# Optimization experiments

Hardware: AMD Instinct MI355X
Metric: run time of the kernel (lower is better)

Reference implementation:

```python
import jax, jax.numpy as jnp
import numpy as np
from jax import lax

WINDOW_SIZE = 11
SIGMA = 1.5
MAX_VAL = 1.0


def _gaussian_kernel_2d(window_size: int, sigma: float) -> jnp.ndarray:
    coords = jnp.arange(window_size, dtype=jnp.float32) - window_size // 2
    g = jnp.exp(-coords ** 2 / (2.0 * sigma ** 2))
    g = g / g.sum()
    k2d = jnp.outer(g, g)
    return k2d / k2d.sum()  # [W, W]


def _depthwise_conv(x: jnp.ndarray, k2d: jnp.ndarray) -> jnp.ndarray:
    # x: [B, C, H, W]; depthwise (groups=C) conv with SAME padding
    C = x.shape[1]
    ws = k2d.shape[0]
    kernel = jnp.broadcast_to(k2d[None, None], (C, 1, ws, ws)).astype(x.dtype)  # [C,1,ws,ws]
    pad = ws // 2
    return lax.conv_general_dilated(
        x, kernel,
        window_strides=(1, 1),
        padding=((pad, pad), (pad, pad)),
        dimension_numbers=('NCHW', 'OIHW', 'NCHW'),
        feature_group_count=C,
    )


def setup_inputs() -> dict:
    key = jax.random.key(0)
    k1, k2 = jax.random.split(key)
    B, C, H, W = 16, 3, 512, 512
    sr = jax.random.uniform(k1, (B, C, H, W), dtype=jnp.float32)
    hr = jax.random.uniform(k2, (B, C, H, W), dtype=jnp.float32)
    return {"sr": sr, "hr": hr}


def reference(sr, hr):
    c1 = (0.01 * MAX_VAL) ** 2
    c2 = (0.03 * MAX_VAL) ** 2
    k2d = _gaussian_kernel_2d(WINDOW_SIZE, SIGMA)

    mu1 = _depthwise_conv(sr, k2d)
    mu2 = _depthwise_conv(hr, k2d)
    mu1_sq = mu1 ** 2
    mu2_sq = mu2 ** 2
    mu1_mu2 = mu1 * mu2
    sigma1_sq = _depthwise_conv(sr * sr, k2d) - mu1_sq
    sigma2_sq = _depthwise_conv(hr * hr, k2d) - mu2_sq
    sigma12 = _depthwise_conv(sr * hr, k2d) - mu1_mu2

    ssim_map = (2 * mu1_mu2 + c1) * (2 * sigma12 + c2) / (
        (mu1_sq + mu2_sq + c1) * (sigma1_sq + sigma2_sq + c2) + 1e-12)
    return 1.0 - ssim_map.mean()
```

## Files before the change

### kernel.cpp

```cpp
#include <hip/hip_runtime.h>


typedef __attribute__((ext_vector_type(2))) float  f32x2;
typedef __attribute__((ext_vector_type(4))) float  f32x4;
typedef __fp16 f16;
typedef __attribute__((ext_vector_type(2))) __fp16 h2v;
typedef __attribute__((ext_vector_type(4))) __fp16 h4;
typedef __attribute__((ext_vector_type(8))) __fp16 h8;

constexpr int IMG_H = 512;
constexpr int IMG_W = 512;
constexpr int NBC   = 48;
constexpr int TW    = 64;
constexpr int TH    = 32;
constexpr int NBLKX = IMG_W / TW;
constexpr int NBLKY = IMG_H / TH;
constexpr int NBLK  = NBLKX * NBLKY * NBC;

constexpr int XP   = 104;
constexpr int XR   = 48;
constexpr int XQS  = XR * XP;
constexpr int HTP  = 72;
constexpr int HTQS = 64 * HTP;
constexpr int SMEMH = 4 * XQS;
static_assert(4 * HTQS <= SMEMH, "Ht must fit in X union");

constexpr float C1 = 1.0e-4f;
constexpr float C2 = 9.0e-4f;

__device__ const float GW[11] = {
    0.00102838f, 0.00759876f, 0.03600077f, 0.10936070f, 0.21300553f,
    0.26601172f, 0.21300553f, 0.10936070f, 0.03600077f, 0.00759876f,
    0.00102838f};

__device__ __forceinline__ h8 ldfrag(const f16* __restrict__ gtab, int base) {
    h8 b;
#pragma unroll
    for (int i = 0; i < 8; ++i) b[i] = gtab[base + i];
    return b;
}

__global__ __launch_bounds__(64) void ssim_init(double* acc) {
    if (threadIdx.x == 0) acc[0] = 0.0;
}

__global__ __launch_bounds__(256, 4) void ssim_main(const float* __restrict__ sr,
                                                    const float* __restrict__ hr,
                                                    double* __restrict__ sink,
                                                    int mode) {
    __shared__ __align__(16) f16 smem[SMEMH];
    __shared__ __align__(8)  f16 gtab[128];
    __shared__ float wsums[4];

    const int tid  = threadIdx.x;
    const int w    = tid >> 6;
    const int lane = tid & 63;
    const int l15  = lane & 15;
    const int grp8 = (lane >> 4) << 3;
    const int grp4 = (lane >> 4) << 2;

    const int bc  = blockIdx.z;
    const int gr0 = blockIdx.y * TH - 5;
    const int gc0 = blockIdx.x * TW - 8;
    const float* __restrict__ srp = sr + (size_t)bc * IMG_H * IMG_W;
    const float* __restrict__ hrp = hr + (size_t)bc * IMG_H * IMG_W;

    const int c8  = tid & 15;
    const int r0s = tid >> 4;
    float4 La0[3], La1[3], Lb0[3], Lb1[3];
#pragma unroll
    for (int t = 0; t < 3; ++t) {
        const int r  = r0s + 16 * t;
        const int gr = gr0 + r;
        const int gc = gc0 + c8 * 8;
        La0[t] = La1[t] = Lb0[t] = Lb1[t] = (float4){0.f, 0.f, 0.f, 0.f};
        if ((c8 < 10) & (r < 42) &
            ((unsigned)gr < (unsigned)IMG_H) & ((unsigned)gc < (unsigned)IMG_W)) {
            const float4* pa = (const float4*)&srp[(size_t)gr * IMG_W + gc];
            const float4* pb = (const float4*)&hrp[(size_t)gr * IMG_W + gc];
            La0[t] = pa[0]; La1[t] = pa[1];
            Lb0[t] = pb[0]; Lb1[t] = pb[1];
        }
    }

    if (tid < 128) {
        const int d = tid - 66;
        float v = 0.f;
        if ((unsigned)d <= 10u) v = GW[d];
        gtab[tid] = (f16)v;
    }

    if (c8 < 10) {
#pragma unroll
        for (int t = 0; t < 3; ++t) {
            const int r = r0s + 16 * t;
            const f32x2* a0 = (const f32x2*)&La0[t];
            const f32x2* a1 = (const f32x2*)&La1[t];
            const f32x2* b0 = (const f32x2*)&Lb0[t];
            const f32x2* b1 = (const f32x2*)&Lb1[t];
            const f32x2 s0 = a0[0] * a0[0] + b0[0] * b0[0];
            const f32x2 s1 = a0[1] * a0[1] + b0[1] * b0[1];
            const f32x2 s2 = a1[0] * a1[0] + b1[0] * b1[0];
            const f32x2 s3 = a1[1] * a1[1] + b1[1] * b1[1];
            const f32x2 p0 = a0[0] * b0[0], p1 = a0[1] * b0[1];
            const f32x2 p2 = a1[0] * b1[0], p3 = a1[1] * b1[1];
            union { h2v h2[4]; h8 v; } uva, uvb, uss, uab;
            uva.h2[0] = __builtin_amdgcn_cvt_pkrtz(a0[0].x, a0[0].y);
            uva.h2[1] = __builtin_amdgcn_cvt_pkrtz(a0[1].x, a0[1].y);
            uva.h2[2] = __builtin_amdgcn_cvt_pkrtz(a1[0].x, a1[0].y);
            uva.h2[3] = __builtin_amdgcn_cvt_pkrtz(a1[1].x, a1[1].y);
            uvb.h2[0] = __builtin_amdgcn_cvt_pkrtz(b0[0].x, b0[0].y);
            uvb.h2[1] = __builtin_amdgcn_cvt_pkrtz(b0[1].x, b0[1].y);
            uvb.h2[2] = __builtin_amdgcn_cvt_pkrtz(b1[0].x, b1[0].y);
            uvb.h2[3] = __builtin_amdgcn_cvt_pkrtz(b1[1].x, b1[1].y);
            uss.h2[0] = __builtin_amdgcn_cvt_pkrtz(s0.x, s0.y);
            uss.h2[1] = __builtin_amdgcn_cvt_pkrtz(s1.x, s1.y);
            uss.h2[2] = __builtin_amdgcn_cvt_pkrtz(s2.x, s2.y);
            uss.h2[3] = __builtin_amdgcn_cvt_pkrtz(s3.x, s3.y);
            uab.h2[0] = __builtin_amdgcn_cvt_pkrtz(p0.x, p0.y);
            uab.h2[1] = __builtin_amdgcn_cvt_pkrtz(p1.x, p1.y);
            uab.h2[2] = __builtin_amdgcn_cvt_pkrtz(p2.x, p2.y);
            uab.h2[3] = __builtin_amdgcn_cvt_pkrtz(p3.x, p3.y);
            const int o = r * XP + c8 * 8;
            *(h8*)&smem[0 * XQS + o] = uva.v;
            *(h8*)&smem[1 * XQS + o] = uvb.v;
            *(h8*)&smem[2 * XQS + o] = uss.v;
            *(h8*)&smem[3 * XQS + o] = uab.v;
        }
    }
    __syncthreads();

    float s16 = 0.f;
#pragma unroll
    for (int d = 0; d <= 10; ++d) s16 += (float)gtab[66 + d];
    const float rs = 1.0f / (s16 * s16);

    const h8 bh = ldfrag(gtab, 63 + grp8 - l15);
    f32x4 acc[4][3] = {};
#pragma unroll
    for (int Mt = 0; Mt < 3; ++Mt) {
        const int arow = (16 * Mt + l15) * XP + 16 * w + grp8;
#pragma unroll
        for (int q = 0; q < 4; ++q) {
            const h8 af = *(const h8*)&smem[q * XQS + arow];
            acc[q][Mt] = __builtin_amdgcn_mfma_f32_16x16x32_f16(af, bh, acc[q][Mt], 0, 0, 0);
        }
    }
    __syncthreads();

#pragma unroll
    for (int q = 0; q < 4; ++q) {
#pragma unroll
        for (int Mt = 0; Mt < 3; ++Mt) {
            union { h2v h2[2]; h4 v; } u;
            u.h2[0] = __builtin_amdgcn_cvt_pkrtz(acc[q][Mt][0], acc[q][Mt][1]);
            u.h2[1] = __builtin_amdgcn_cvt_pkrtz(acc[q][Mt][2], acc[q][Mt][3]);
            *(h4*)&smem[q * HTQS + (16 * w + l15) * HTP + 16 * Mt + grp4] = u.v;
        }
    }

    const h8 bv = ldfrag(gtab, 66 + grp8 - l15);
    f32x4 acc2[4][2] = {};
    const int abase = (16 * w + l15) * HTP + grp8;
#pragma unroll
    for (int q = 0; q < 4; ++q) {
        const h8 a0 = *(const h8*)&smem[q * HTQS + abase];
        const h8 a1 = *(const h8*)&smem[q * HTQS + abase + 16];
        acc2[q][0] = __builtin_amdgcn_mfma_f32_16x16x32_f16(a0, bv, acc2[q][0], 0, 0, 0);
        acc2[q][1] = __builtin_amdgcn_mfma_f32_16x16x32_f16(a1, bv, acc2[q][1], 0, 0, 0);
    }

    float local = 0.f;
#pragma unroll
    for (int nt = 0; nt < 2; ++nt) {
        const f32x4 m1 = acc2[0][nt] * rs;
        const f32x4 m2 = acc2[1][nt] * rs;
        const f32x4 S  = acc2[2][nt] * rs;
        const f32x4 pp = acc2[3][nt] * rs;
        const f32x4 mu1s = m1 * m1, mu2s = m2 * m2, mu12 = m1 * m2;
        const f32x4 sg12 = pp - mu12;
        const f32x4 sgs  = S - mu1s - mu2s;
        const f32x4 num = (2.f * mu12 + C1) * (2.f * sg12 + C2);
        const f32x4 den = (mu1s + mu2s + C1) * (sgs + C2) + 1e-12f;
#pragma unroll
        for (int e = 0; e < 4; ++e)
            local += num[e] * __builtin_amdgcn_rcpf(den[e]);
    }

#pragma unroll
    for (int off = 32; off > 0; off >>= 1)
        local += __shfl_down(local, off, 64);
    if ((tid & 63) == 0) wsums[tid >> 6] = local;
    __syncthreads();
    if (tid == 0) {
        const double bsum = (double)(wsums[0] + wsums[1] + wsums[2] + wsums[3]);
        if (mode == 0) {
            const int bid = (blockIdx.z * NBLKY + blockIdx.y) * NBLKX + blockIdx.x;
            sink[bid] = bsum;
        } else {
            atomicAdd(sink, bsum);
        }
    }
}

__global__ __launch_bounds__(256) void ssim_finalize(const double* __restrict__ partial,
                                                     float* __restrict__ out, int count) {
    __shared__ double ws[4];
    double s = 0.0;
    for (int i = threadIdx.x; i < count; i += 256) s += partial[i];
#pragma unroll
    for (int off = 32; off > 0; off >>= 1)
        s += __shfl_down(s, off, 64);
    const int lane = threadIdx.x & 63, wave = threadIdx.x >> 6;
    if (lane == 0) ws[wave] = s;
    __syncthreads();
    if (threadIdx.x == 0) {
        const double tot = ws[0] + ws[1] + ws[2] + ws[3];
        const double n = (double)NBC * IMG_H * IMG_W;
        out[0] = (float)(1.0 - tot / n);
    }
}

extern "C" void kernel_launch(void* const* d_in, const int* in_sizes, int n_in,
                              void* d_out, int out_size, void* d_ws, size_t ws_size,
                              hipStream_t stream) {
    const float* sr = (const float*)d_in[0];
    const float* hr = (const float*)d_in[1];
    float* out = (float*)d_out;
    const dim3 grid(NBLKX, NBLKY, NBC);

    if (ws_size >= (size_t)NBLK * sizeof(double)) {
        double* partial = (double*)d_ws;
        ssim_main<<<grid, dim3(256), 0, stream>>>(sr, hr, partial, 0);
        ssim_finalize<<<dim3(1), dim3(256), 0, stream>>>(partial, out, NBLK);
    } else {
        double* acc = (double*)d_ws;
        ssim_init<<<dim3(1), dim3(64), 0, stream>>>(acc);
        ssim_main<<<grid, dim3(256), 0, stream>>>(sr, hr, acc, 1);
        ssim_finalize<<<dim3(1), dim3(256), 0, stream>>>(acc, out, 1);
    }
}
```

Baseline: 133.9 us.

## Make main kernel persistent with register prefetch of next tile across planes

Replaces the 6144-block grid with 1024 persistent blocks. Each block loops over 6 planes at the same spatial tile, stepping 8 planes each iteration. The global loads for the next plane are issued into registers after the shared-memory stage and before the MFMA work, so load latency overlaps compute. This also cuts the number of partial sums and the finalize work, at the cost of an extra barrier per iteration and fewer resident blocks for latency hiding.

```diff
diff --git a/kernel.cpp b/kernel.cpp
--- a/kernel.cpp
+++ b/kernel.cpp
@@ -10,12 +10,14 @@
 
 constexpr int IMG_H = 512;
 constexpr int IMG_W = 512;
+constexpr int PL    = IMG_H * IMG_W;
 constexpr int NBC   = 48;
 constexpr int TW    = 64;
 constexpr int TH    = 32;
 constexpr int NBLKX = IMG_W / TW;
 constexpr int NBLKY = IMG_H / TH;
-constexpr int NBLK  = NBLKX * NBLKY * NBC;
+constexpr int NPERS = 1024;
+constexpr int ITERS = NBLKX * NBLKY * NBC / NPERS;
 
 constexpr int XP   = 104;
 constexpr int XR   = 48;
@@ -59,28 +61,29 @@
     const int grp8 = (lane >> 4) << 3;
     const int grp4 = (lane >> 4) << 2;
 
-    const int bc  = blockIdx.z;
-    const int gr0 = blockIdx.y * TH - 5;
-    const int gc0 = blockIdx.x * TW - 8;
-    const float* __restrict__ srp = sr + (size_t)bc * IMG_H * IMG_W;
-    const float* __restrict__ hrp = hr + (size_t)bc * IMG_H * IMG_W;
+    const int bx  = blockIdx.x & 7;
+    const int by  = (blockIdx.x >> 3) & 15;
+    const int bc0 = blockIdx.x >> 7;
+    const int gr0 = by * TH - 5;
+    const int gc0 = bx * TW - 8;
+
+    const float* __restrict__ srp = sr + (size_t)bc0 * PL;
+    const float* __restrict__ hrp = hr + (size_t)bc0 * PL;
+    const size_t PSTEP = (size_t)8 * PL;
 
     const int c8  = tid & 15;
     const int r0s = tid >> 4;
-    float4 La0[3], La1[3], Lb0[3], Lb1[3];
+    unsigned okm = 0;
+    int off[3];
 #pragma unroll
     for (int t = 0; t < 3; ++t) {
         const int r  = r0s + 16 * t;
         const int gr = gr0 + r;
         const int gc = gc0 + c8 * 8;
-        La0[t] = La1[t] = Lb0[t] = Lb1[t] = (float4){0.f, 0.f, 0.f, 0.f};
         if ((c8 < 10) & (r < 42) &
-            ((unsigned)gr < (unsigned)IMG_H) & ((unsigned)gc < (unsigned)IMG_W)) {
-            const float4* pa = (const float4*)&srp[(size_t)gr * IMG_W + gc];
-            const float4* pb = (const float4*)&hrp[(size_t)gr * IMG_W + gc];
-            La0[t] = pa[0]; La1[t] = pa[1];
-            Lb0[t] = pb[0]; Lb1[t] = pb[1];
-        }
+            ((unsigned)gr < (unsigned)IMG_H) & ((unsigned)gc < (unsigned)IMG_W))
+            okm |= (1u << t);
+        off[t] = gr * IMG_W + gc;
     }
 
     if (tid < 128) {
@@ -90,113 +93,143 @@
         gtab[tid] = (f16)v;
     }
 
-    if (c8 < 10) {
-#pragma unroll
-        for (int t = 0; t < 3; ++t) {
-            const int r = r0s + 16 * t;
-            const f32x2* a0 = (const f32x2*)&La0[t];
-            const f32x2* a1 = (const f32x2*)&La1[t];
-            const f32x2* b0 = (const f32x2*)&Lb0[t];
-            const f32x2* b1 = (const f32x2*)&Lb1[t];
-            const f32x2 s0 = a0[0] * a0[0] + b0[0] * b0[0];
-            const f32x2 s1 = a0[1] * a0[1] + b0[1] * b0[1];
-            const f32x2 s2 = a1[0] * a1[0] + b1[0] * b1[0];
-            const f32x2 s3 = a1[1] * a1[1] + b1[1] * b1[1];
-            const f32x2 p0 = a0[0] * b0[0], p1 = a0[1] * b0[1];
-            const f32x2 p2 = a1[0] * b1[0], p3 = a1[1] * b1[1];
-            union { h2v h2[4]; h8 v; } uva, uvb, uss, uab;
-            uva.h2[0] = __builtin_amdgcn_cvt_pkrtz(a0[0].x, a0[0].y);
-            uva.h2[1] = __builtin_amdgcn_cvt_pkrtz(a0[1].x, a0[1].y);
-            uva.h2[2] = __builtin_amdgcn_cvt_pkrtz(a1[0].x, a1[0].y);
-            uva.h2[3] = __builtin_amdgcn_cvt_pkrtz(a1[1].x, a1[1].y);
-            uvb.h2[0] = __builtin_amdgcn_cvt_pkrtz(b0[0].x, b0[0].y);
-            uvb.h2[1] = __builtin_amdgcn_cvt_pkrtz(b0[1].x, b0[1].y);
-            uvb.h2[2] = __builtin_amdgcn_cvt_pkrtz(b1[0].x, b1[0].y);
-            uvb.h2[3] = __builtin_amdgcn_cvt_pkrtz(b1[1].x, b1[1].y);
-            uss.h2[0] = __builtin_amdgcn_cvt_pkrtz(s0.x, s0.y);
-            uss.h2[1] = __builtin_amdgcn_cvt_pkrtz(s1.x, s1.y);
-            uss.h2[2] = __builtin_amdgcn_cvt_pkrtz(s2.x, s2.y);
-            uss.h2[3] = __builtin_amdgcn_cvt_pkrtz(s3.x, s3.y);
-            uab.h2[0] = __builtin_amdgcn_cvt_pkrtz(p0.x, p0.y);
-            uab.h2[1] = __builtin_amdgcn_cvt_pkrtz(p1.x, p1.y);
-            uab.h2[2] = __builtin_amdgcn_cvt_pkrtz(p2.x, p2.y);
-            uab.h2[3] = __builtin_amdgcn_cvt_pkrtz(p3.x, p3.y);
-            const int o = r * XP + c8 * 8;
-            *(h8*)&smem[0 * XQS + o] = uva.v;
-            *(h8*)&smem[1 * XQS + o] = uvb.v;
-            *(h8*)&smem[2 * XQS + o] = uss.v;
-            *(h8*)&smem[3 * XQS + o] = uab.v;
+    float s16 = 0.f;
+#pragma unroll
+    for (int d = 0; d <= 10; ++d) s16 += (float)(f16)GW[d];
+    const float rs = 1.0f / (s16 * s16);
+
+    float4 La0[3], La1[3], Lb0[3], Lb1[3];
+#pragma unroll
+    for (int t = 0; t < 3; ++t) {
+        La0[t] = La1[t] = Lb0[t] = Lb1[t] = (float4){0.f, 0.f, 0.f, 0.f};
+        if (okm & (1u << t)) {
+            const float4* pa = (const float4*)&srp[off[t]];
+            const float4* pb = (const float4*)&hrp[off[t]];
+            La0[t] = pa[0]; La1[t] = pa[1];
+            Lb0[t] = pb[0]; Lb1[t] = pb[1];
         }
     }
     __syncthreads();
 
-    float s16 = 0.f;
-#pragma unroll
-    for (int d = 0; d <= 10; ++d) s16 += (float)gtab[66 + d];
-    const float rs = 1.0f / (s16 * s16);
-
     const h8 bh = ldfrag(gtab, 63 + grp8 - l15);
-    f32x4 acc[4][3] = {};
-#pragma unroll
-    for (int Mt = 0; Mt < 3; ++Mt) {
-        const int arow = (16 * Mt + l15) * XP + 16 * w + grp8;
+    const h8 bv = ldfrag(gtab, 66 + grp8 - l15);
+
+    float local = 0.f;
+
+    for (int iter = 0; iter < ITERS; ++iter) {
+        if (c8 < 10) {
+#pragma unroll
+            for (int t = 0; t < 3; ++t) {
+                const int r = r0s + 16 * t;
+                const f32x2* a0 = (const f32x2*)&La0[t];
+                const f32x2* a1 = (const f32x2*)&La1[t];
+                const f32x2* b0 = (const f32x2*)&Lb0[t];
+                const f32x2* b1 = (const f32x2*)&Lb1[t];
+                const f32x2 s0 = a0[0] * a0[0] + b0[0] * b0[0];
+                const f32x2 s1 = a0[1] * a0[1] + b0[1] * b0[1];
+                const f32x2 s2 = a1[0] * a1[0] + b1[0] * b1[0];
+                const f32x2 s3 = a1[1] * a1[1] + b1[1] * b1[1];
+                const f32x2 p0 = a0[0] * b0[0], p1 = a0[1] * b0[1];
+                const f32x2 p2 = a1[0] * b1[0], p3 = a1[1] * b1[1];
+                union { h2v h2[4]; h8 v; } uva, uvb, uss, uab;
+                uva.h2[0] = __builtin_amdgcn_cvt_pkrtz(a0[0].x, a0[0].y);
+                uva.h2[1] = __builtin_amdgcn_cvt_pkrtz(a0[1].x, a0[1].y);
+                uva.h2[2] = __builtin_amdgcn_cvt_pkrtz(a1[0].x, a1[0].y);
+                uva.h2[3] = __builtin_amdgcn_cvt_pkrtz(a1[1].x, a1[1].y);
+                uvb.h2[0] = __builtin_amdgcn_cvt_pkrtz(b0[0].x, b0[0].y);
+                uvb.h2[1] = __builtin_amdgcn_cvt_pkrtz(b0[1].x, b0[1].y);
+                uvb.h2[2] = __builtin_amdgcn_cvt_pkrtz(b1[0].x, b1[0].y);
+                uvb.h2[3] = __builtin_amdgcn_cvt_pkrtz(b1[1].x, b1[1].y);
+                uss.h2[0] = __builtin_amdgcn_cvt_pkrtz(s0.x, s0.y);
+                uss.h2[1] = __builtin_amdgcn_cvt_pkrtz(s1.x, s1.y);
+                uss.h2[2] = __builtin_amdgcn_cvt_pkrtz(s2.x, s2.y);
+                uss.h2[3] = __builtin_amdgcn_cvt_pkrtz(s3.x, s3.y);
+                uab.h2[0] = __builtin_amdgcn_cvt_pkrtz(p0.x, p0.y);
+                uab.h2[1] = __builtin_amdgcn_cvt_pkrtz(p1.x, p1.y);
+                uab.h2[2] = __builtin_amdgcn_cvt_pkrtz(p2.x, p2.y);
+                uab.h2[3] = __builtin_amdgcn_cvt_pkrtz(p3.x, p3.y);
+                const int o = r * XP + c8 * 8;
+                *(h8*)&smem[0 * XQS + o] = uva.v;
+                *(h8*)&smem[1 * XQS + o] = uvb.v;
+                *(h8*)&smem[2 * XQS + o] = uss.v;
+                *(h8*)&smem[3 * XQS + o] = uab.v;
+            }
+        }
+        __syncthreads();
+
+        if (iter < ITERS - 1) {
+            srp += PSTEP; hrp += PSTEP;
+#pragma unroll
+            for (int t = 0; t < 3; ++t) {
+                if (okm & (1u << t)) {
+                    const float4* pa = (const float4*)&srp[off[t]];
+                    const float4* pb = (const float4*)&hrp[off[t]];
+                    La0[t] = pa[0]; La1[t] = pa[1];
+                    Lb0[t] = pb[0]; Lb1[t] = pb[1];
+                }
+            }
+        }
+
+        f32x4 acc[4][3] = {};
+#pragma unroll
+        for (int Mt = 0; Mt < 3; ++Mt) {
+            const int arow = (16 * Mt + l15) * XP + 16 * w + grp8;
+#pragma unroll
+            for (int q = 0; q < 4; ++q) {
+                const h8 af = *(const h8*)&smem[q * XQS + arow];
+                acc[q][Mt] = __builtin_amdgcn_mfma_f32_16x16x32_f16(af, bh, acc[q][Mt], 0, 0, 0);
+            }
+        }
+        __syncthreads();
+
 #pragma unroll
         for (int q = 0; q < 4; ++q) {
-            const h8 af = *(const h8*)&smem[q * XQS + arow];
-            acc[q][Mt] = __builtin_amdgcn_mfma_f32_16x16x32_f16(af, bh, acc[q][Mt], 0, 0, 0);
-        }
-    }
-    __syncthreads();
-
-#pragma unroll
-    for (int q = 0; q < 4; ++q) {
-#pragma unroll
-        for (int Mt = 0; Mt < 3; ++Mt) {
-            union { h2v h2[2]; h4 v; } u;
-            u.h2[0] = __builtin_amdgcn_cvt_pkrtz(acc[q][Mt][0], acc[q][Mt][1]);
-            u.h2[1] = __builtin_amdgcn_cvt_pkrtz(acc[q][Mt][2], acc[q][Mt][3]);
-            *(h4*)&smem[q * HTQS + (16 * w + l15) * HTP + 16 * Mt + grp4] = u.v;
-        }
-    }
-
-    const h8 bv = ldfrag(gtab, 66 + grp8 - l15);
-    f32x4 acc2[4][2] = {};
-    const int abase = (16 * w + l15) * HTP + grp8;
-#pragma unroll
-    for (int q = 0; q < 4; ++q) {
-        const h8 a0 = *(const h8*)&smem[q * HTQS + abase];
-        const h8 a1 = *(const h8*)&smem[q * HTQS + abase + 16];
-        acc2[q][0] = __builtin_amdgcn_mfma_f32_16x16x32_f16(a0, bv, acc2[q][0], 0, 0, 0);
-        acc2[q][1] = __builtin_amdgcn_mfma_f32_16x16x32_f16(a1, bv, acc2[q][1], 0, 0, 0);
-    }
-
-    float local = 0.f;
-#pragma unroll
-    for (int nt = 0; nt < 2; ++nt) {
-        const f32x4 m1 = acc2[0][nt] * rs;
-        const f32x4 m2 = acc2[1][nt] * rs;
-        const f32x4 S  = acc2[2][nt] * rs;
-        const f32x4 pp = acc2[3][nt] * rs;
-        const f32x4 mu1s = m1 * m1, mu2s = m2 * m2, mu12 = m1 * m2;
-        const f32x4 sg12 = pp - mu12;
-        const f32x4 sgs  = S - mu1s - mu2s;
-        const f32x4 num = (2.f * mu12 + C1) * (2.f * sg12 + C2);
-        const f32x4 den = (mu1s + mu2s + C1) * (sgs + C2) + 1e-12f;
-#pragma unroll
-        for (int e = 0; e < 4; ++e)
-            local += num[e] * __builtin_amdgcn_rcpf(den[e]);
-    }
-
-#pragma unroll
-    for (int off = 32; off > 0; off >>= 1)
-        local += __shfl_down(local, off, 64);
+#pragma unroll
+            for (int Mt = 0; Mt < 3; ++Mt) {
+                union { h2v h2[2]; h4 v; } u;
+                u.h2[0] = __builtin_amdgcn_cvt_pkrtz(acc[q][Mt][0], acc[q][Mt][1]);
+                u.h2[1] = __builtin_amdgcn_cvt_pkrtz(acc[q][Mt][2], acc[q][Mt][3]);
+                *(h4*)&smem[q * HTQS + (16 * w + l15) * HTP + 16 * Mt + grp4] = u.v;
+            }
+        }
+
+        f32x4 acc2[4][2] = {};
+        const int abase = (16 * w + l15) * HTP + grp8;
+#pragma unroll
+        for (int q = 0; q < 4; ++q) {
+            const h8 a0 = *(const h8*)&smem[q * HTQS + abase];
+            const h8 a1 = *(const h8*)&smem[q * HTQS + abase + 16];
+            acc2[q][0] = __builtin_amdgcn_mfma_f32_16x16x32_f16(a0, bv, acc2[q][0], 0, 0, 0);
+            acc2[q][1] = __builtin_amdgcn_mfma_f32_16x16x32_f16(a1, bv, acc2[q][1], 0, 0, 0);
+        }
+
+#pragma unroll
+        for (int nt = 0; nt < 2; ++nt) {
+            const f32x4 m1 = acc2[0][nt] * rs;
+            const f32x4 m2 = acc2[1][nt] * rs;
+            const f32x4 S  = acc2[2][nt] * rs;
+            const f32x4 pp = acc2[3][nt] * rs;
+            const f32x4 mu1s = m1 * m1, mu2s = m2 * m2, mu12 = m1 * m2;
+            const f32x4 sg12 = pp - mu12;
+            const f32x4 sgs  = S - mu1s - mu2s;
+            const f32x4 num = (2.f * mu12 + C1) * (2.f * sg12 + C2);
+            const f32x4 den = (mu1s + mu2s + C1) * (sgs + C2) + 1e-12f;
+#pragma unroll
+            for (int e = 0; e < 4; ++e)
+                local += num[e] * __builtin_amdgcn_rcpf(den[e]);
+        }
+        __syncthreads();
+    }
+
+#pragma unroll
+    for (int offr = 32; offr > 0; offr >>= 1)
+        local += __shfl_down(local, offr, 64);
     if ((tid & 63) == 0) wsums[tid >> 6] = local;
     __syncthreads();
     if (tid == 0) {
         const double bsum = (double)(wsums[0] + wsums[1] + wsums[2] + wsums[3]);
         if (mode == 0) {
-            const int bid = (blockIdx.z * NBLKY + blockIdx.y) * NBLKX + blockIdx.x;
-            sink[bid] = bsum;
+            sink[blockIdx.x] = bsum;
         } else {
             atomicAdd(sink, bsum);
         }
@@ -227,16 +260,15 @@
     const float* sr = (const float*)d_in[0];
     const float* hr = (const float*)d_in[1];
     float* out = (float*)d_out;
-    const dim3 grid(NBLKX, NBLKY, NBC);
-
-    if (ws_size >= (size_t)NBLK * sizeof(double)) {
+
+    if (ws_size >= (size_t)NPERS * sizeof(double)) {
         double* partial = (double*)d_ws;
-        ssim_main<<<grid, dim3(256), 0, stream>>>(sr, hr, partial, 0);
-        ssim_finalize<<<dim3(1), dim3(256), 0, stream>>>(partial, out, NBLK);
+        ssim_main<<<dim3(NPERS), dim3(256), 0, stream>>>(sr, hr, partial, 0);
+        ssim_finalize<<<dim3(1), dim3(256), 0, stream>>>(partial, out, NPERS);
     } else {
         double* acc = (double*)d_ws;
         ssim_init<<<dim3(1), dim3(64), 0, stream>>>(acc);
-        ssim_main<<<grid, dim3(256), 0, stream>>>(sr, hr, acc, 1);
+        ssim_main<<<dim3(NPERS), dim3(256), 0, stream>>>(sr, hr, acc, 1);
         ssim_finalize<<<dim3(1), dim3(256), 0, stream>>>(acc, out, 1);
     }
 }
```

Measured after the change: 130.0 us. -2.9%, faster.
